# Kernel tuning notes

Measured on AMD Instinct MI355X. Metric: run time of the kernel, lower is better.

The kernel has to match this reference:

```python
import jax, jax.numpy as jnp
import numpy as np

D = 384
MAXPOS = 6

def setup_inputs() -> dict:
    key = jax.random.key(0)
    ks = jax.random.split(key, 20)
    B, Lt, Lh, E = 4, 1024, 512, 64
    inp = {
        'text': jax.random.normal(ks[0], (B, Lt, D), jnp.float32),
        'html': jax.random.normal(ks[1], (B, Lh, D), jnp.float32),
        'H2Hmask': jax.random.randint(ks[2], (B, Lh, Lh), 0, E, jnp.int32),
        'T2Tmask': (jax.random.uniform(ks[3], (B, Lt, Lt)) < 0.1).astype(jnp.float32),
        'H2Tmask': (jax.random.uniform(ks[4], (B, Lh, Lt)) < 0.1).astype(jnp.float32),
        'T2Hmask': (jax.random.uniform(ks[5], (B, Lt, Lh)) < 0.1).astype(jnp.float32),
        'positionembedding': jax.random.normal(ks[6], (2 * MAXPOS + 1, D), jnp.float32) * 0.02,
        'htmledgeembedding': jax.random.normal(ks[7], (E, D), jnp.float32) * 0.02,
    }
    names = ['W_V_T', 'W_V_H', 'W_Q_H2H', 'W_K_H2H', 'W_Q_H2T', 'W_K_H2T',
             'W_Q_T2H', 'W_K_T2H', 'W_Q_T2T', 'W_K_T2T']
    lim = np.sqrt(6.0 / (D + D))  # glorot_uniform
    for i, n in enumerate(names):
        inp[n] = jax.random.uniform(ks[8 + i], (D, D), jnp.float32, -lim, lim)
    return inp


def _forward(text, html, H2Hmask, T2Tmask, H2Tmask, T2Hmask,
             positionembedding, htmledgeembedding,
             W_V_T, W_V_H, W_Q_H2H, W_K_H2H, W_Q_H2T, W_K_H2T,
             W_Q_T2H, W_K_T2H, W_Q_T2T, W_K_T2T):
    B, Lt, _ = text.shape
    Lh = html.shape[1]
    scale = 1.0 / jnp.sqrt(jnp.float32(D))

    text_v = text @ W_V_T   # (B,Lt,D)
    html_v = html @ W_V_H   # (B,Lh,D)

    # ---- H2H: content + gathered edge-embedding bias ----
    # sum_d q[b,i,d] * (k[b,j,d] + edge[H2Hmask[b,i,j], d])
    #   = (q k^T)[b,i,j] + (q E^T)[b,i, H2Hmask[b,i,j]]
    h2h_q = html @ W_Q_H2H
    h2h_k = html @ W_K_H2H
    h2h_content = jnp.einsum('bid,bjd->bij', h2h_q, h2h_k)
    qe = h2h_q @ htmledgeembedding.T                       # (B,Lh,E)
    h2h_bias = jnp.take_along_axis(qe, H2Hmask, axis=-1)   # (B,Lh,Lh)
    h2h_e = (h2h_content + h2h_bias) * scale
    h2h_e = h2h_e - 10000.0 * (H2Hmask == 0).astype(jnp.float32)
    html1 = jax.nn.softmax(h2h_e, axis=-1) @ html_v

    # ---- H2T ----
    h2t_e = jnp.einsum('bid,bjd->bij', html @ W_Q_H2T, text @ W_K_H2T) * scale
    h2t_e = h2t_e - 10000.0 * H2Tmask
    html2 = jax.nn.softmax(h2t_e, axis=-1) @ text_v

    # ---- T2H (note: original code never applies T2Hmask) ----
    t2h_e = jnp.einsum('bid,bjd->bij', text @ W_Q_T2H, html @ W_K_T2H) * scale
    text1 = jax.nn.softmax(t2h_e, axis=-1) @ html_v

    # ---- T2T: content + relative-position bias ----
    idx = jnp.arange(Lt, dtype=jnp.int32)
    pos_ids = jnp.clip(idx[None, :] - idx[:, None], -MAXPOS, MAXPOS) + MAXPOS  # (Lt,Lt)
    t2t_q = text @ W_Q_T2T
    t2t_k = text @ W_K_T2T
    t2t_content = jnp.einsum('bid,bjd->bij', t2t_q, t2t_k)
    qp = t2t_q @ positionembedding.T                       # (B,Lt,2*MAXPOS+1)
    t2t_bias = jnp.take_along_axis(
        qp, jnp.broadcast_to(pos_ids[None], (B, Lt, Lt)), axis=-1)
    t2t_e = (t2t_content + t2t_bias) * scale
    t2t_e = t2t_e - 10000.0 * T2Tmask
    text2 = jax.nn.softmax(t2t_e, axis=-1) @ text_v

    # concat updated text (Lt) and html (Lh) along seq axis -> (B, Lt+Lh, D)
    return jnp.concatenate([text1 + text2, html1 + html2], axis=1)


def reference(text, html, H2Hmask, T2Tmask, H2Tmask, T2Hmask,
              positionembedding, htmledgeembedding,
              W_V_T, W_V_H, W_Q_H2H, W_K_H2H, W_Q_H2T, W_K_H2T,
              W_Q_T2H, W_K_T2H, W_Q_T2T, W_K_T2T):
    return _forward(text, html, H2Hmask, T2Tmask, H2Tmask, T2Hmask,
                    positionembedding, htmledgeembedding,
                    W_V_T, W_V_H, W_Q_H2H, W_K_H2H, W_Q_H2T, W_K_H2T,
                    W_Q_T2H, W_K_T2H, W_Q_T2T, W_K_T2T)
```

## Files before the change

### kernel.cpp

```cpp
#include <hip/hip_runtime.h>
#include <math.h>

typedef unsigned short u16;
typedef unsigned int u32;
typedef __attribute__((ext_vector_type(8))) short short8;
typedef __attribute__((ext_vector_type(4))) float f32x4;

__device__ __forceinline__ u16 f2bf(float f) {
    u32 u = __float_as_uint(f);
    u = (u + 0x7FFFu + ((u >> 16) & 1u)) >> 16;
    return (u16)u;
}
__device__ __forceinline__ float bf2f(u16 h) {
    return __uint_as_float(((u32)h) << 16);
}
__device__ __forceinline__ float4 ld4f(const float* p) {
    return *reinterpret_cast<const float4*>(p);
}


__global__ __launch_bounds__(256)
void cvt2(const float4* __restrict__ a, int na4,
          const float4* __restrict__ b, int nb4,
          u16* __restrict__ oa, u16* __restrict__ ob)
{
    int idx = blockIdx.x * 256 + threadIdx.x;
    const int tot = na4 + nb4;
    for (; idx < tot; idx += gridDim.x * 256) {
        float4 v; u16* o;
        if (idx < na4) { v = a[idx];        o = oa + (long)idx * 4; }
        else           { v = b[idx - na4];  o = ob + (long)(idx - na4) * 4; }
        u32 lo = (u32)f2bf(v.x) | ((u32)f2bf(v.y) << 16);
        u32 hi = (u32)f2bf(v.z) | ((u32)f2bf(v.w) << 16);
        uint2 pk; pk.x = lo; pk.y = hi;
        *reinterpret_cast<uint2*>(o) = pk;
    }
}

struct WP { const float* p[10]; };
struct WD { u16* d[10]; };

__global__ __launch_bounds__(1024)
void wtrans(WP w, WD wd)
{
    __shared__ float t[32][33];
    const int z = blockIdx.z;
    const float* W = w.p[z];
    const int k = blockIdx.x * 32 + threadIdx.y;
    const int n = blockIdx.y * 32 + threadIdx.x;
    t[threadIdx.y][threadIdx.x] = W[k * 384 + n];
    __syncthreads();
    const int no = blockIdx.y * 32 + threadIdx.y;
    const int ko = blockIdx.x * 32 + threadIdx.x;
    wd.d[z][no * 384 + ko] = f2bf(t[threadIdx.x][threadIdx.y]);
}

__device__ __forceinline__ void mfma_core64(
    const u16* __restrict__ A, int lda,
    const u16* __restrict__ B, int ldb, int K,
    u16 (&As)[2][4096], u16 (&Bs)[2][4096],
    f32x4 (&acc)[2][2])
{
    const int tid  = threadIdx.x;
    const int wid  = tid >> 6;
    const int lane = tid & 63;
    const int wr = wid >> 1, wc = wid & 1;
    const int lane15 = lane & 15;
    const int lq = lane >> 4;
    const int g0 = wid * 64 + lane;

    #pragma unroll
    for (int i = 0; i < 2; ++i)
        #pragma unroll
        for (int j = 0; j < 2; ++j)
            acc[i][j] = (f32x4){0.f, 0.f, 0.f, 0.f};

    auto stage = [&](const u16* __restrict__ G, int ld, int k0, u16* lds) {
        #pragma unroll
        for (int h = 0; h < 2; ++h) {
            const int gid  = g0 + h * 256;
            const int row  = gid >> 3;
            const int slot = (gid & 7) ^ (row & 7);
            const u16* src = G + (long)row * ld + k0 + slot * 8;
            u16* dst = lds + wid * 512 + h * 2048;
            __builtin_amdgcn_global_load_lds(
                (const __attribute__((address_space(1))) void*)src,
                (__attribute__((address_space(3))) void*)dst, 16, 0, 0);
        }
    };
    auto rd = [&](const u16* lds, int row, int colslot) -> short8 {
        const int byt = row * 128 + ((colslot ^ (row & 7)) << 4);
        return *reinterpret_cast<const short8*>(
            reinterpret_cast<const char*>(lds) + byt);
    };

    stage(A, lda, 0, As[0]);
    stage(B, ldb, 0, Bs[0]);
    __syncthreads();

    const int nt = K >> 6;
    int cur = 0;
    for (int t = 0; t < nt; ++t) {
        if (t + 1 < nt) {
            stage(A, lda, (t + 1) << 6, As[cur ^ 1]);
            stage(B, ldb, (t + 1) << 6, Bs[cur ^ 1]);
        }
        short8 af[2][2], bf[2][2];
        #pragma unroll
        for (int mi = 0; mi < 2; ++mi)
            #pragma unroll
            for (int kk = 0; kk < 2; ++kk)
                af[mi][kk] = rd(As[cur], wr * 32 + mi * 16 + lane15, kk * 4 + lq);
        #pragma unroll
        for (int ni = 0; ni < 2; ++ni)
            #pragma unroll
            for (int kk = 0; kk < 2; ++kk)
                bf[ni][kk] = rd(Bs[cur], wc * 32 + ni * 16 + lane15, kk * 4 + lq);
        #pragma unroll
        for (int mi = 0; mi < 2; ++mi)
            #pragma unroll
            for (int ni = 0; ni < 2; ++ni)
                #pragma unroll
                for (int kk = 0; kk < 2; ++kk)
                    acc[mi][ni] = __builtin_amdgcn_mfma_f32_16x16x32_bf16(
                        af[mi][kk], bf[ni][kk], acc[mi][ni], 0, 0, 0);
        __syncthreads();
        cur ^= 1;
    }
}

struct Seg {
    const u16* A; const u16* B; float* C;
    long sA, sB, sC;
    int lda, ldb, ldc, K, nbx, nbxSh, start, pad;
};
struct Segs { Seg s[4]; };

template<int NSEG>
__global__ __launch_bounds__(256)
void gemm_grouped(Segs d)
{
    __shared__ __align__(16) u16 As[2][4096];
    __shared__ __align__(16) u16 Bs[2][4096];
    const int bid = blockIdx.x;
    Seg sg = d.s[0];
    if (NSEG > 1 && bid >= d.s[1].start) sg = d.s[1];
    if (NSEG > 2 && bid >= d.s[2].start) sg = d.s[2];
    if (NSEG > 3 && bid >= d.s[3].start) sg = d.s[3];

    const int local = bid - sg.start;
    const int bx = local & (sg.nbx - 1);
    const int by = local >> sg.nbxSh;
    const int z  = blockIdx.y;
    const int m0 = bx * 64, n0 = by * 64;

    const u16* A = sg.A + (long)z * sg.sA + (long)m0 * sg.lda;
    const u16* B = sg.B + (long)z * sg.sB + (long)n0 * sg.ldb;

    f32x4 acc[2][2];
    mfma_core64(A, sg.lda, B, sg.ldb, sg.K, As, Bs, acc);

    const int tid = threadIdx.x;
    const int wid = tid >> 6, lane = tid & 63;
    const int wr = wid >> 1, wc = wid & 1;
    const int lane15 = lane & 15;
    const int r0 = (lane >> 4) * 4;

    float* C = sg.C + (long)z * sg.sC;
    #pragma unroll
    for (int mi = 0; mi < 2; ++mi)
        #pragma unroll
        for (int r = 0; r < 4; ++r) {
            const int row = m0 + wr * 32 + mi * 16 + r0 + r;
            float* crow = C + (long)row * sg.ldc + n0 + wc * 32 + lane15;
            #pragma unroll
            for (int ni = 0; ni < 2; ++ni)
                crow[ni * 16] = acc[mi][ni][r];
        }
}

struct PSeg {
    const u16* A; const u16* Bw; u16* QK; u16* VT;
    int lvtSh, vtOff, nbx, nbxSh, start, pad;
};
struct PSegs { PSeg s[2]; };

__global__ __launch_bounds__(256)
void proj_grouped(PSegs d)
{
    __shared__ __align__(16) u16 As[2][4096];
    __shared__ __align__(16) u16 Bs[2][4096];
    const int bid = blockIdx.x;
    PSeg sg = d.s[0];
    if (bid >= d.s[1].start) sg = d.s[1];

    const int local = bid - sg.start;
    const int bx = local & (sg.nbx - 1);
    const int by = local >> sg.nbxSh;
    const int m0 = bx * 64, n0 = by * 64;

    const u16* A = sg.A + (long)m0 * 384;
    const u16* B = sg.Bw + (long)n0 * 384;

    f32x4 acc[2][2];
    mfma_core64(A, 384, B, 384, 384, As, Bs, acc);

    const int tid = threadIdx.x;
    const int wid = tid >> 6, lane = tid & 63;
    const int wr = wid >> 1, wc = wid & 1;
    const int lane15 = lane & 15;
    const int r0 = (lane >> 4) * 4;
    const int lmask = (1 << sg.lvtSh) - 1;

    if (n0 < 384) {
        #pragma unroll
        for (int mi = 0; mi < 2; ++mi) {
            const int row = m0 + wr * 32 + mi * 16 + r0;
            const int bz = row >> sg.lvtSh;
            const int l  = row & lmask;
            #pragma unroll
            for (int ni = 0; ni < 2; ++ni) {
                const int col = n0 + wc * 32 + ni * 16 + lane15;
                u32 lo = (u32)f2bf(acc[mi][ni][0]) | ((u32)f2bf(acc[mi][ni][1]) << 16);
                u32 hi = (u32)f2bf(acc[mi][ni][2]) | ((u32)f2bf(acc[mi][ni][3]) << 16);
                uint2 pk; pk.x = lo; pk.y = hi;
                *reinterpret_cast<uint2*>(
                    sg.VT + ((long)bz * 384 + col) * 1536 + sg.vtOff + l) = pk;
            }
        }
    } else {
        #pragma unroll
        for (int mi = 0; mi < 2; ++mi)
            #pragma unroll
            for (int r = 0; r < 4; ++r) {
                const int row = m0 + wr * 32 + mi * 16 + r0 + r;
                u16* qrow = sg.QK + (long)row * 1536 + (n0 - 384) + wc * 32 + lane15;
                #pragma unroll
                for (int ni = 0; ni < 2; ++ni)
                    qrow[ni * 16] = f2bf(acc[mi][ni][r]);
            }
    }
}

__global__ __launch_bounds__(256)
void gemm_bias2(const u16* __restrict__ A0, const float* __restrict__ B0,
                float* __restrict__ C0, int N0,
                const u16* __restrict__ A1, const float* __restrict__ B1,
                float* __restrict__ C1, int N1)
{
    __shared__ float As[16][64];
    __shared__ float Bs[16][64];
    const int bid = blockIdx.x;
    const u16* A; const float* B; float* C; int N, m0;
    if (bid < 32) { A = A0; B = B0; C = C0; N = N0; m0 = bid * 64; }
    else          { A = A1; B = B1; C = C1; N = N1; m0 = (bid - 32) * 64; }

    const int tid = threadIdx.x;
    const int tx = tid & 15, ty = tid >> 4;
    const int ar = tid >> 2;
    const int ak = (tid & 3) << 2;

    float acc[4][4] = {{0.f,0.f,0.f,0.f},{0.f,0.f,0.f,0.f},
                       {0.f,0.f,0.f,0.f},{0.f,0.f,0.f,0.f}};

    for (int k0 = 0; k0 < 384; k0 += 16) {
        const u16* ap = A + (long)(m0 + ar) * 1536 + (k0 + ak);
        ushort4 a4 = *reinterpret_cast<const ushort4*>(ap);
        As[ak+0][ar] = bf2f(a4.x); As[ak+1][ar] = bf2f(a4.y);
        As[ak+2][ar] = bf2f(a4.z); As[ak+3][ar] = bf2f(a4.w);

        float4 bv = make_float4(0.f,0.f,0.f,0.f);
        if (ar < N) bv = ld4f(B + (long)ar * 384 + (k0 + ak));
        Bs[ak+0][ar] = bv.x; Bs[ak+1][ar] = bv.y;
        Bs[ak+2][ar] = bv.z; Bs[ak+3][ar] = bv.w;
        __syncthreads();

        #pragma unroll
        for (int kk = 0; kk < 16; ++kk) {
            float4 af = ld4f(&As[kk][ty * 4]);
            float4 bfv = ld4f(&Bs[kk][tx * 4]);
            float a[4] = {af.x, af.y, af.z, af.w};
            float b[4] = {bfv.x, bfv.y, bfv.z, bfv.w};
            #pragma unroll
            for (int i = 0; i < 4; ++i)
                #pragma unroll
                for (int j = 0; j < 4; ++j)
                    acc[i][j] = fmaf(a[i], b[j], acc[i][j]);
        }
        __syncthreads();
    }
    #pragma unroll
    for (int i = 0; i < 4; ++i) {
        const int row = m0 + ty * 4 + i;
        float* crow = C + (long)row * N;
        #pragma unroll
        for (int j = 0; j < 4; ++j) {
            const int col = tx * 4 + j;
            if (col < N) crow[col] = acc[i][j];
        }
    }
}


__device__ __forceinline__ float blockReduceMax(float v, float* red, int tid) {
    #pragma unroll
    for (int o = 32; o >= 1; o >>= 1) v = fmaxf(v, __shfl_xor(v, o));
    if ((tid & 63) == 0) red[tid >> 6] = v;
    __syncthreads();
    return fmaxf(fmaxf(red[0], red[1]), fmaxf(red[2], red[3]));
}
__device__ __forceinline__ float blockReduceSum(float v, float* red, int tid) {
    #pragma unroll
    for (int o = 32; o >= 1; o >>= 1) v += __shfl_xor(v, o);
    if ((tid & 63) == 0) red[4 + (tid >> 6)] = v;
    __syncthreads();
    return red[4] + red[5] + red[6] + red[7];
}

__global__ __launch_bounds__(256)
void softmax_fused(const float* __restrict__ scoresH, u16* __restrict__ probsH,
                   const float* __restrict__ scoresT, u16* __restrict__ probsT,
                   const float* __restrict__ qe, const float* __restrict__ qp,
                   const int* __restrict__ H2Hmask,
                   const float* __restrict__ H2Tmask,
                   const float* __restrict__ T2Tmask, float scale)
{
    const int bid = blockIdx.x;
    const int tid = threadIdx.x;
    __shared__ float qsh[64];
    __shared__ float red[8];

    if (bid < 2048) {
        const int b = bid >> 9, i = bid & 511;
        const long rbase = ((long)b * 512 + i) * 1536;
        const float* rowS = scoresH + rbase;
        u16* rowP = probsH + rbase;
        const int*   mrow  = H2Hmask + ((long)b * 512 + i) * 512;
        const float* m2row = H2Tmask + ((long)b * 512 + i) * 1024;
        if (tid < 64) qsh[tid] = qe[((long)b * 512 + i) * 64 + tid];
        __syncthreads();

        float x[2]; float mx = -1e30f;
        #pragma unroll
        for (int t = 0; t < 2; ++t) {
            const int j = tid + t * 256;
            const int m = mrow[j];
            float v = (rowS[j] + qsh[m]) * scale - 10000.f * (m == 0 ? 1.f : 0.f);
            x[t] = v; mx = fmaxf(mx, v);
        }
        mx = blockReduceMax(mx, red, tid);
        float s = 0.f;
        #pragma unroll
        for (int t = 0; t < 2; ++t) { x[t] = __expf(x[t] - mx); s += x[t]; }
        s = blockReduceSum(s, red, tid);
        float inv = 1.f / s;
        #pragma unroll
        for (int t = 0; t < 2; ++t) rowP[tid + t * 256] = f2bf(x[t] * inv);

        float y[4]; mx = -1e30f;
        #pragma unroll
        for (int t = 0; t < 4; ++t) {
            const int jj = tid + t * 256;
            float v = rowS[512 + jj] * scale - 10000.f * m2row[jj];
            y[t] = v; mx = fmaxf(mx, v);
        }
        mx = blockReduceMax(mx, red, tid);
        s = 0.f;
        #pragma unroll
        for (int t = 0; t < 4; ++t) { y[t] = __expf(y[t] - mx); s += y[t]; }
        s = blockReduceSum(s, red, tid);
        inv = 1.f / s;
        #pragma unroll
        for (int t = 0; t < 4; ++t) rowP[512 + tid + t * 256] = f2bf(y[t] * inv);
    } else {
        const int bid2 = bid - 2048;
        const int b = bid2 >> 10, i = bid2 & 1023;
        const long rbase = ((long)b * 1024 + i) * 1536;
        const float* rowS = scoresT + rbase;
        u16* rowP = probsT + rbase;
        const float* m2row = T2Tmask + ((long)b * 1024 + i) * 1024;
        if (tid < 13) qsh[tid] = qp[((long)b * 1024 + i) * 13 + tid];
        __syncthreads();

        float x[2]; float mx = -1e30f;
        #pragma unroll
        for (int t = 0; t < 2; ++t) {
            const int j = tid + t * 256;
            float v = rowS[j] * scale;
            x[t] = v; mx = fmaxf(mx, v);
        }
        mx = blockReduceMax(mx, red, tid);
        float s = 0.f;
        #pragma unroll
        for (int t = 0; t < 2; ++t) { x[t] = __expf(x[t] - mx); s += x[t]; }
        s = blockReduceSum(s, red, tid);
        float inv = 1.f / s;
        #pragma unroll
        for (int t = 0; t < 2; ++t) rowP[tid + t * 256] = f2bf(x[t] * inv);

        float y[4]; mx = -1e30f;
        #pragma unroll
        for (int t = 0; t < 4; ++t) {
            const int jj = tid + t * 256;
            int pos = jj - i;
            pos = (pos < -6 ? -6 : (pos > 6 ? 6 : pos)) + 6;
            float v = (rowS[512 + jj] + qsh[pos]) * scale - 10000.f * m2row[jj];
            y[t] = v; mx = fmaxf(mx, v);
        }
        mx = blockReduceMax(mx, red, tid);
        s = 0.f;
        #pragma unroll
        for (int t = 0; t < 4; ++t) { y[t] = __expf(y[t] - mx); s += y[t]; }
        s = blockReduceSum(s, red, tid);
        inv = 1.f / s;
        #pragma unroll
        for (int t = 0; t < 4; ++t) rowP[512 + tid + t * 256] = f2bf(y[t] * inv);
    }
}


extern "C" void kernel_launch(void* const* d_in, const int* in_sizes, int n_in,
                              void* d_out, int out_size, void* d_ws, size_t ws_size,
                              hipStream_t stream)
{
    const int Bn = 4, Lt = 1024, Lh = 512, Dd = 384;
    const float scale = 0.05103103630798288f;

    const float* text    = (const float*)d_in[0];
    const float* html    = (const float*)d_in[1];
    const int*   H2Hmask = (const int*)  d_in[2];
    const float* T2Tmask = (const float*)d_in[3];
    const float* H2Tmask = (const float*)d_in[4];
    const float* posemb  = (const float*)d_in[6];
    const float* edgeemb = (const float*)d_in[7];
    float* out = (float*)d_out;

    char* p = (char*)d_ws;
    auto au16 = [&](long n) { u16* r = (u16*)p;  p += ((n * 2 + 255) & ~255L); return r; };
    auto af32 = [&](long n) { float* r = (float*)p; p += ((n * 4 + 255) & ~255L); return r; };

    const long nT = (long)Bn * Lt * Dd;
    const long nH = (long)Bn * Lh * Dd;
    u16* text_bf = au16(nT);
    u16* html_bf = au16(nH);
    u16* WTtext  = au16(5L * 384 * 384);
    u16* WThtml  = au16(5L * 384 * 384);
    u16* textQK  = au16((long)Bn * Lt * 1536);
    u16* htmlQK  = au16((long)Bn * Lh * 1536);
    u16* VTs     = au16((long)Bn * 384 * 1536);
    float* qe = af32((long)Bn * Lh * 64);
    float* qp = af32((long)Bn * Lt * 13);
    float* scoresH = af32((long)Bn * Lh * 1536);
    float* scoresT = af32((long)Bn * Lt * 1536);
    u16* probsH = au16((long)Bn * Lh * 1536);
    u16* probsT = au16((long)Bn * Lt * 1536);

    cvt2<<<2048, 256, 0, stream>>>((const float4*)text, (int)(nT / 4),
                                   (const float4*)html, (int)(nH / 4),
                                   text_bf, html_bf);
    WP wp; WD wd;
    for (int i = 0; i < 10; ++i) wp.p[i] = (const float*)d_in[8 + i];
    const long WSZ = 147456;
    wd.d[0] = WTtext + 0 * WSZ;
    wd.d[1] = WThtml + 0 * WSZ;
    wd.d[2] = WThtml + 1 * WSZ;
    wd.d[3] = WThtml + 2 * WSZ;
    wd.d[4] = WThtml + 3 * WSZ;
    wd.d[5] = WTtext + 1 * WSZ;
    wd.d[6] = WTtext + 2 * WSZ;
    wd.d[7] = WThtml + 4 * WSZ;
    wd.d[8] = WTtext + 3 * WSZ;
    wd.d[9] = WTtext + 4 * WSZ;
    wtrans<<<dim3(12, 12, 10), dim3(32, 32), 0, stream>>>(wp, wd);

    u16* h2h_q = htmlQK + 0;     u16* h2h_k = htmlQK + 384;
    u16* h2t_q = htmlQK + 768;   u16* t2h_k = htmlQK + 1152;
    u16* h2t_k = textQK + 0;     u16* t2h_q = textQK + 384;
    u16* t2t_q = textQK + 768;   u16* t2t_k = textQK + 1152;

    PSegs pj;
    pj.s[0] = { text_bf, WTtext, textQK, VTs, 10, 512, 64, 6, 0,    0 };
    pj.s[1] = { html_bf, WThtml, htmlQK, VTs,  9,   0, 32, 5, 1920, 0 };
    proj_grouped<<<2880, 256, 0, stream>>>(pj);

    gemm_bias2<<<96, 256, 0, stream>>>(h2h_q, edgeemb, qe, 64,
                                       t2t_q, posemb,  qp, 13);

    const long sQt = (long)Lt * 1536, sQh = (long)Lh * 1536;
    const long sSh = (long)Lh * 1536, sSt = (long)Lt * 1536;
    const long sV  = (long)384 * 1536;
    const long sOut = (long)(Lt + Lh) * 384;

    Segs sc;
    sc.s[0] = { h2h_q, h2h_k, scoresH,       sQh, sQh, sSh, 1536, 1536, 1536, 384,  8, 3,   0, 0 };
    sc.s[1] = { h2t_q, h2t_k, scoresH + 512, sQh, sQt, sSh, 1536, 1536, 1536, 384,  8, 3,  64, 0 };
    sc.s[2] = { t2h_q, t2h_k, scoresT,       sQt, sQh, sSt, 1536, 1536, 1536, 384, 16, 4, 192, 0 };
    sc.s[3] = { t2t_q, t2t_k, scoresT + 512, sQt, sQt, sSt, 1536, 1536, 1536, 384, 16, 4, 320, 0 };
    gemm_grouped<4><<<dim3(576, 4), 256, 0, stream>>>(sc);

    softmax_fused<<<6144, 256, 0, stream>>>(scoresH, probsH, scoresT, probsT,
                                            qe, qp, H2Hmask, H2Tmask, T2Tmask,
                                            scale);

    Segs pv;
    pv.s[0] = { probsH, VTs, out + (long)Lt * 384, sQh, sV, sOut, 1536, 1536, 384, 1536,  8, 3,  0, 0 };
    pv.s[1] = { probsT, VTs, out,                  sQt, sV, sOut, 1536, 1536, 384, 1536, 16, 4, 48, 0 };
    pv.s[2] = pv.s[1]; pv.s[3] = pv.s[1];
    gemm_grouped<2><<<dim3(144, 4), 256, 0, stream>>>(pv);
}
```

Before: 215.9 us.

## Use 128x128 MFMA tiles and fold bias GEMMs into grouped score GEMM

The MFMA GEMM core moves from 64x64 tiles with a double-buffered, XOR-swizzled K=64 pipeline to 128x128 tiles with a single-buffered K=32 loop. Each wave now computes 4x4 fragments, which raises arithmetic intensity per LDS load. The separate scalar-FMA gemm_bias2 kernel is removed. The edge and position embeddings are converted to bf16 and padded to 128 rows, and the q·E^T and q·P^T products run as two extra segments of the grouped score GEMM. This cuts one launch and reuses the tensor-core path, but drops the load/compute overlap and leaves LDS reads unswizzled, so bank conflicts are likely. It also launches far fewer blocks, which may underfill the GPU.

```diff
diff --git a/kernel.cpp b/kernel.cpp
--- a/kernel.cpp
+++ b/kernel.cpp
@@ -14,22 +14,25 @@
 __device__ __forceinline__ float bf2f(u16 h) {
     return __uint_as_float(((u32)h) << 16);
 }
-__device__ __forceinline__ float4 ld4f(const float* p) {
-    return *reinterpret_cast<const float4*>(p);
-}
 
 
 __global__ __launch_bounds__(256)
-void cvt2(const float4* __restrict__ a, int na4,
+void cvt4(const float4* __restrict__ a, int na4,
           const float4* __restrict__ b, int nb4,
-          u16* __restrict__ oa, u16* __restrict__ ob)
+          const float4* __restrict__ c, int nc4,
+          const float4* __restrict__ d, int nd4,
+          u16* __restrict__ oa, u16* __restrict__ ob,
+          u16* __restrict__ oc, u16* __restrict__ od)
 {
     int idx = blockIdx.x * 256 + threadIdx.x;
-    const int tot = na4 + nb4;
+    const int tot = na4 + nb4 + nc4 + nd4;
     for (; idx < tot; idx += gridDim.x * 256) {
         float4 v; u16* o;
-        if (idx < na4) { v = a[idx];        o = oa + (long)idx * 4; }
-        else           { v = b[idx - na4];  o = ob + (long)(idx - na4) * 4; }
+        int t = idx;
+        if (t < na4)      { v = a[t]; o = oa + (long)t * 4; }
+        else if ((t -= na4) < nb4) { v = b[t]; o = ob + (long)t * 4; }
+        else if ((t -= nb4) < nc4) { v = c[t]; o = oc + (long)t * 4; }
+        else { t -= nc4;    v = d[t]; o = od + (long)t * 4; }
         u32 lo = (u32)f2bf(v.x) | ((u32)f2bf(v.y) << 16);
         u32 hi = (u32)f2bf(v.z) | ((u32)f2bf(v.w) << 16);
         uint2 pk; pk.x = lo; pk.y = hi;
@@ -55,77 +58,60 @@
     wd.d[z][no * 384 + ko] = f2bf(t[threadIdx.x][threadIdx.y]);
 }
 
-__device__ __forceinline__ void mfma_core64(
+__device__ __forceinline__ void mfma_core128(
     const u16* __restrict__ A, int lda,
     const u16* __restrict__ B, int ldb, int K,
-    u16 (&As)[2][4096], u16 (&Bs)[2][4096],
-    f32x4 (&acc)[2][2])
+    u16* __restrict__ As, u16* __restrict__ Bs,
+    f32x4 (&acc)[4][4])
 {
     const int tid  = threadIdx.x;
     const int wid  = tid >> 6;
     const int lane = tid & 63;
     const int wr = wid >> 1, wc = wid & 1;
     const int lane15 = lane & 15;
-    const int lq = lane >> 4;
-    const int g0 = wid * 64 + lane;
+    const int kg = (lane >> 4) * 8;
+    const int srow = lane >> 2;
+    const int scol = (lane & 3) * 8;
 
     #pragma unroll
-    for (int i = 0; i < 2; ++i)
-        #pragma unroll
-        for (int j = 0; j < 2; ++j)
+    for (int i = 0; i < 4; ++i)
+        #pragma unroll
+        for (int j = 0; j < 4; ++j)
             acc[i][j] = (f32x4){0.f, 0.f, 0.f, 0.f};
 
-    auto stage = [&](const u16* __restrict__ G, int ld, int k0, u16* lds) {
-        #pragma unroll
-        for (int h = 0; h < 2; ++h) {
-            const int gid  = g0 + h * 256;
-            const int row  = gid >> 3;
-            const int slot = (gid & 7) ^ (row & 7);
-            const u16* src = G + (long)row * ld + k0 + slot * 8;
-            u16* dst = lds + wid * 512 + h * 2048;
+    for (int k0 = 0; k0 < K; k0 += 32) {
+        #pragma unroll
+        for (int i = 0; i < 2; ++i) {
+            const int rg = (wid * 2 + i) * 16;
+            const u16* ga = A + (long)(rg + srow) * lda + (k0 + scol);
+            const u16* gb = B + (long)(rg + srow) * ldb + (k0 + scol);
+            u16* la = As + (wid * 2 + i) * 512;
+            u16* lb = Bs + (wid * 2 + i) * 512;
             __builtin_amdgcn_global_load_lds(
-                (const __attribute__((address_space(1))) void*)src,
-                (__attribute__((address_space(3))) void*)dst, 16, 0, 0);
-        }
-    };
-    auto rd = [&](const u16* lds, int row, int colslot) -> short8 {
-        const int byt = row * 128 + ((colslot ^ (row & 7)) << 4);
-        return *reinterpret_cast<const short8*>(
-            reinterpret_cast<const char*>(lds) + byt);
-    };
-
-    stage(A, lda, 0, As[0]);
-    stage(B, ldb, 0, Bs[0]);
-    __syncthreads();
-
-    const int nt = K >> 6;
-    int cur = 0;
-    for (int t = 0; t < nt; ++t) {
-        if (t + 1 < nt) {
-            stage(A, lda, (t + 1) << 6, As[cur ^ 1]);
-            stage(B, ldb, (t + 1) << 6, Bs[cur ^ 1]);
-        }
-        short8 af[2][2], bf[2][2];
-        #pragma unroll
-        for (int mi = 0; mi < 2; ++mi)
+                (const __attribute__((address_space(1))) void*)ga,
+                (__attribute__((address_space(3))) void*)la, 16, 0, 0);
+            __builtin_amdgcn_global_load_lds(
+                (const __attribute__((address_space(1))) void*)gb,
+                (__attribute__((address_space(3))) void*)lb, 16, 0, 0);
+        }
+        __syncthreads();
+
+        short8 af[4], bf[4];
+        #pragma unroll
+        for (int mi = 0; mi < 4; ++mi)
+            af[mi] = *reinterpret_cast<const short8*>(
+                As + (wr * 64 + mi * 16 + lane15) * 32 + kg);
+        #pragma unroll
+        for (int ni = 0; ni < 4; ++ni)
+            bf[ni] = *reinterpret_cast<const short8*>(
+                Bs + (wc * 64 + ni * 16 + lane15) * 32 + kg);
+        #pragma unroll
+        for (int mi = 0; mi < 4; ++mi)
             #pragma unroll
-            for (int kk = 0; kk < 2; ++kk)
-                af[mi][kk] = rd(As[cur], wr * 32 + mi * 16 + lane15, kk * 4 + lq);
-        #pragma unroll
-        for (int ni = 0; ni < 2; ++ni)
-            #pragma unroll
-            for (int kk = 0; kk < 2; ++kk)
-                bf[ni][kk] = rd(Bs[cur], wc * 32 + ni * 16 + lane15, kk * 4 + lq);
-        #pragma unroll
-        for (int mi = 0; mi < 2; ++mi)
-            #pragma unroll
-            for (int ni = 0; ni < 2; ++ni)
-                #pragma unroll
-                for (int kk = 0; kk < 2; ++kk)
-                    acc[mi][ni] = __builtin_amdgcn_mfma_f32_16x16x32_bf16(
-                        af[mi][kk], bf[ni][kk], acc[mi][ni], 0, 0, 0);
+            for (int ni = 0; ni < 4; ++ni)
+                acc[mi][ni] = __builtin_amdgcn_mfma_f32_16x16x32_bf16(
+                    af[mi], bf[ni], acc[mi][ni], 0, 0, 0);
         __syncthreads();
-        cur ^= 1;
     }
 }
 
@@ -134,31 +120,33 @@
     long sA, sB, sC;
     int lda, ldb, ldc, K, nbx, nbxSh, start, pad;
 };
-struct Segs { Seg s[4]; };
+struct Segs { Seg s[6]; };
 
 template<int NSEG>
 __global__ __launch_bounds__(256)
 void gemm_grouped(Segs d)
 {
-    __shared__ __align__(16) u16 As[2][4096];
-    __shared__ __align__(16) u16 Bs[2][4096];
+    __shared__ __align__(16) u16 As[4096];
+    __shared__ __align__(16) u16 Bs[4096];
     const int bid = blockIdx.x;
     Seg sg = d.s[0];
     if (NSEG > 1 && bid >= d.s[1].start) sg = d.s[1];
     if (NSEG > 2 && bid >= d.s[2].start) sg = d.s[2];
     if (NSEG > 3 && bid >= d.s[3].start) sg = d.s[3];
+    if (NSEG > 4 && bid >= d.s[4].start) sg = d.s[4];
+    if (NSEG > 5 && bid >= d.s[5].start) sg = d.s[5];
 
     const int local = bid - sg.start;
     const int bx = local & (sg.nbx - 1);
     const int by = local >> sg.nbxSh;
     const int z  = blockIdx.y;
-    const int m0 = bx * 64, n0 = by * 64;
+    const int m0 = bx * 128, n0 = by * 128;
 
     const u16* A = sg.A + (long)z * sg.sA + (long)m0 * sg.lda;
     const u16* B = sg.B + (long)z * sg.sB + (long)n0 * sg.ldb;
 
-    f32x4 acc[2][2];
-    mfma_core64(A, sg.lda, B, sg.ldb, sg.K, As, Bs, acc);
+    f32x4 acc[4][4];
+    mfma_core128(A, sg.lda, B, sg.ldb, sg.K, As, Bs, acc);
 
     const int tid = threadIdx.x;
     const int wid = tid >> 6, lane = tid & 63;
@@ -168,13 +156,13 @@
 
     float* C = sg.C + (long)z * sg.sC;
     #pragma unroll
-    for (int mi = 0; mi < 2; ++mi)
+    for (int mi = 0; mi < 4; ++mi)
         #pragma unroll
         for (int r = 0; r < 4; ++r) {
-            const int row = m0 + wr * 32 + mi * 16 + r0 + r;
-            float* crow = C + (long)row * sg.ldc + n0 + wc * 32 + lane15;
+            const int row = m0 + wr * 64 + mi * 16 + r0 + r;
+            float* crow = C + (long)row * sg.ldc + n0 + wc * 64 + lane15;
             #pragma unroll
-            for (int ni = 0; ni < 2; ++ni)
+            for (int ni = 0; ni < 4; ++ni)
                 crow[ni * 16] = acc[mi][ni][r];
         }
 }
@@ -188,8 +176,8 @@
 __global__ __launch_bounds__(256)
 void proj_grouped(PSegs d)
 {
-    __shared__ __align__(16) u16 As[2][4096];
-    __shared__ __align__(16) u16 Bs[2][4096];
+    __shared__ __align__(16) u16 As[4096];
+    __shared__ __align__(16) u16 Bs[4096];
     const int bid = blockIdx.x;
     PSeg sg = d.s[0];
     if (bid >= d.s[1].start) sg = d.s[1];
@@ -197,13 +185,13 @@
     const int local = bid - sg.start;
     const int bx = local & (sg.nbx - 1);
     const int by = local >> sg.nbxSh;
-    const int m0 = bx * 64, n0 = by * 64;
+    const int m0 = bx * 128, n0 = by * 128;
 
     const u16* A = sg.A + (long)m0 * 384;
     const u16* B = sg.Bw + (long)n0 * 384;
 
-    f32x4 acc[2][2];
-    mfma_core64(A, 384, B, 384, 384, As, Bs, acc);
+    f32x4 acc[4][4];
+    mfma_core128(A, 384, B, 384, 384, As, Bs, acc);
 
     const int tid = threadIdx.x;
     const int wid = tid >> 6, lane = tid & 63;
@@ -214,13 +202,13 @@
 
     if (n0 < 384) {
         #pragma unroll
-        for (int mi = 0; mi < 2; ++mi) {
-            const int row = m0 + wr * 32 + mi * 16 + r0;
+        for (int mi = 0; mi < 4; ++mi) {
+            const int row = m0 + wr * 64 + mi * 16 + r0;
             const int bz = row >> sg.lvtSh;
             const int l  = row & lmask;
             #pragma unroll
-            for (int ni = 0; ni < 2; ++ni) {
-                const int col = n0 + wc * 32 + ni * 16 + lane15;
+            for (int ni = 0; ni < 4; ++ni) {
+                const int col = n0 + wc * 64 + ni * 16 + lane15;
                 u32 lo = (u32)f2bf(acc[mi][ni][0]) | ((u32)f2bf(acc[mi][ni][1]) << 16);
                 u32 hi = (u32)f2bf(acc[mi][ni][2]) | ((u32)f2bf(acc[mi][ni][3]) << 16);
                 uint2 pk; pk.x = lo; pk.y = hi;
@@ -230,74 +218,15 @@
         }
     } else {
         #pragma unroll
-        for (int mi = 0; mi < 2; ++mi)
+        for (int mi = 0; mi < 4; ++mi)
             #pragma unroll
             for (int r = 0; r < 4; ++r) {
-                const int row = m0 + wr * 32 + mi * 16 + r0 + r;
-                u16* qrow = sg.QK + (long)row * 1536 + (n0 - 384) + wc * 32 + lane15;
+                const int row = m0 + wr * 64 + mi * 16 + r0 + r;
+                u16* qrow = sg.QK + (long)row * 1536 + (n0 - 384) + wc * 64 + lane15;
                 #pragma unroll
-                for (int ni = 0; ni < 2; ++ni)
+                for (int ni = 0; ni < 4; ++ni)
                     qrow[ni * 16] = f2bf(acc[mi][ni][r]);
             }
-    }
-}
-
-__global__ __launch_bounds__(256)
-void gemm_bias2(const u16* __restrict__ A0, const float* __restrict__ B0,
-                float* __restrict__ C0, int N0,
-                const u16* __restrict__ A1, const float* __restrict__ B1,
-                float* __restrict__ C1, int N1)
-{
-    __shared__ float As[16][64];
-    __shared__ float Bs[16][64];
-    const int bid = blockIdx.x;
-    const u16* A; const float* B; float* C; int N, m0;
-    if (bid < 32) { A = A0; B = B0; C = C0; N = N0; m0 = bid * 64; }
-    else          { A = A1; B = B1; C = C1; N = N1; m0 = (bid - 32) * 64; }
-
-    const int tid = threadIdx.x;
-    const int tx = tid & 15, ty = tid >> 4;
-    const int ar = tid >> 2;
-    const int ak = (tid & 3) << 2;
-
-    float acc[4][4] = {{0.f,0.f,0.f,0.f},{0.f,0.f,0.f,0.f},
-                       {0.f,0.f,0.f,0.f},{0.f,0.f,0.f,0.f}};
-
-    for (int k0 = 0; k0 < 384; k0 += 16) {
-        const u16* ap = A + (long)(m0 + ar) * 1536 + (k0 + ak);
-        ushort4 a4 = *reinterpret_cast<const ushort4*>(ap);
-        As[ak+0][ar] = bf2f(a4.x); As[ak+1][ar] = bf2f(a4.y);
-        As[ak+2][ar] = bf2f(a4.z); As[ak+3][ar] = bf2f(a4.w);
-
-        float4 bv = make_float4(0.f,0.f,0.f,0.f);
-        if (ar < N) bv = ld4f(B + (long)ar * 384 + (k0 + ak));
-        Bs[ak+0][ar] = bv.x; Bs[ak+1][ar] = bv.y;
-        Bs[ak+2][ar] = bv.z; Bs[ak+3][ar] = bv.w;
-        __syncthreads();
-
-        #pragma unroll
-        for (int kk = 0; kk < 16; ++kk) {
-            float4 af = ld4f(&As[kk][ty * 4]);
-            float4 bfv = ld4f(&Bs[kk][tx * 4]);
-            float a[4] = {af.x, af.y, af.z, af.w};
-            float b[4] = {bfv.x, bfv.y, bfv.z, bfv.w};
-            #pragma unroll
-            for (int i = 0; i < 4; ++i)
-                #pragma unroll
-                for (int j = 0; j < 4; ++j)
-                    acc[i][j] = fmaf(a[i], b[j], acc[i][j]);
-        }
-        __syncthreads();
-    }
-    #pragma unroll
-    for (int i = 0; i < 4; ++i) {
-        const int row = m0 + ty * 4 + i;
-        float* crow = C + (long)row * N;
-        #pragma unroll
-        for (int j = 0; j < 4; ++j) {
-            const int col = tx * 4 + j;
-            if (col < N) crow[col] = acc[i][j];
-        }
     }
 }
 
@@ -337,7 +266,7 @@
         u16* rowP = probsH + rbase;
         const int*   mrow  = H2Hmask + ((long)b * 512 + i) * 512;
         const float* m2row = H2Tmask + ((long)b * 512 + i) * 1024;
-        if (tid < 64) qsh[tid] = qe[((long)b * 512 + i) * 64 + tid];
+        if (tid < 64) qsh[tid] = qe[((long)b * 512 + i) * 128 + tid];
         __syncthreads();
 
         float x[2]; float mx = -1e30f;
@@ -379,7 +308,7 @@
         const float* rowS = scoresT + rbase;
         u16* rowP = probsT + rbase;
         const float* m2row = T2Tmask + ((long)b * 1024 + i) * 1024;
-        if (tid < 13) qsh[tid] = qp[((long)b * 1024 + i) * 13 + tid];
+        if (tid < 13) qsh[tid] = qp[((long)b * 1024 + i) * 128 + tid];
         __syncthreads();
 
         float x[2]; float mx = -1e30f;
@@ -423,7 +352,7 @@
                               void* d_out, int out_size, void* d_ws, size_t ws_size,
                               hipStream_t stream)
 {
-    const int Bn = 4, Lt = 1024, Lh = 512, Dd = 384;
+    const int Bn = 4, Lt = 1024, Lh = 512;
     const float scale = 0.05103103630798288f;
 
     const float* text    = (const float*)d_in[0];
@@ -439,25 +368,29 @@
     auto au16 = [&](long n) { u16* r = (u16*)p;  p += ((n * 2 + 255) & ~255L); return r; };
     auto af32 = [&](long n) { float* r = (float*)p; p += ((n * 4 + 255) & ~255L); return r; };
 
-    const long nT = (long)Bn * Lt * Dd;
-    const long nH = (long)Bn * Lh * Dd;
+    const long nT = (long)Bn * Lt * 384;
+    const long nH = (long)Bn * Lh * 384;
     u16* text_bf = au16(nT);
     u16* html_bf = au16(nH);
     u16* WTtext  = au16(5L * 384 * 384);
     u16* WThtml  = au16(5L * 384 * 384);
+    u16* edge_bf = au16(128L * 384);
+    u16* pos_bf  = au16(128L * 384);
     u16* textQK  = au16((long)Bn * Lt * 1536);
     u16* htmlQK  = au16((long)Bn * Lh * 1536);
     u16* VTs     = au16((long)Bn * 384 * 1536);
-    float* qe = af32((long)Bn * Lh * 64);
-    float* qp = af32((long)Bn * Lt * 13);
+    float* qe = af32((long)Bn * Lh * 128);
+    float* qp = af32((long)Bn * Lt * 128);
     float* scoresH = af32((long)Bn * Lh * 1536);
     float* scoresT = af32((long)Bn * Lt * 1536);
     u16* probsH = au16((long)Bn * Lh * 1536);
     u16* probsT = au16((long)Bn * Lt * 1536);
 
-    cvt2<<<2048, 256, 0, stream>>>((const float4*)text, (int)(nT / 4),
+    cvt4<<<2048, 256, 0, stream>>>((const float4*)text, (int)(nT / 4),
                                    (const float4*)html, (int)(nH / 4),
-                                   text_bf, html_bf);
+                                   (const float4*)edgeemb, 64 * 384 / 4,
+                                   (const float4*)posemb, 13 * 384 / 4,
+                                   text_bf, html_bf, edge_bf, pos_bf);
     WP wp; WD wd;
     for (int i = 0; i < 10; ++i) wp.p[i] = (const float*)d_in[8 + i];
     const long WSZ = 147456;
@@ -479,12 +412,9 @@
     u16* t2t_q = textQK + 768;   u16* t2t_k = textQK + 1152;
 
     PSegs pj;
-    pj.s[0] = { text_bf, WTtext, textQK, VTs, 10, 512, 64, 6, 0,    0 };
-    pj.s[1] = { html_bf, WThtml, htmlQK, VTs,  9,   0, 32, 5, 1920, 0 };
-    proj_grouped<<<2880, 256, 0, stream>>>(pj);
-
-    gemm_bias2<<<96, 256, 0, stream>>>(h2h_q, edgeemb, qe, 64,
-                                       t2t_q, posemb,  qp, 13);
+    pj.s[0] = { text_bf, WTtext, textQK, VTs, 10, 512, 32, 5, 0,   0 };
+    pj.s[1] = { html_bf, WThtml, htmlQK, VTs,  9,   0, 16, 4, 480, 0 };
+    proj_grouped<<<720, 256, 0, stream>>>(pj);
 
     const long sQt = (long)Lt * 1536, sQh = (long)Lh * 1536;
     const long sSh = (long)Lh * 1536, sSt = (long)Lt * 1536;
@@ -492,19 +422,21 @@
     const long sOut = (long)(Lt + Lh) * 384;
 
     Segs sc;
-    sc.s[0] = { h2h_q, h2h_k, scoresH,       sQh, sQh, sSh, 1536, 1536, 1536, 384,  8, 3,   0, 0 };
-    sc.s[1] = { h2t_q, h2t_k, scoresH + 512, sQh, sQt, sSh, 1536, 1536, 1536, 384,  8, 3,  64, 0 };
-    sc.s[2] = { t2h_q, t2h_k, scoresT,       sQt, sQh, sSt, 1536, 1536, 1536, 384, 16, 4, 192, 0 };
-    sc.s[3] = { t2t_q, t2t_k, scoresT + 512, sQt, sQt, sSt, 1536, 1536, 1536, 384, 16, 4, 320, 0 };
-    gemm_grouped<4><<<dim3(576, 4), 256, 0, stream>>>(sc);
+    sc.s[0] = { h2h_q, h2h_k,  scoresH,       sQh, sQh, sSh, 1536, 1536, 1536, 384, 4, 2,   0, 0 };
+    sc.s[1] = { h2t_q, h2t_k,  scoresH + 512, sQh, sQt, sSh, 1536, 1536, 1536, 384, 4, 2,  16, 0 };
+    sc.s[2] = { t2h_q, t2h_k,  scoresT,       sQt, sQh, sSt, 1536, 1536, 1536, 384, 8, 3,  48, 0 };
+    sc.s[3] = { t2t_q, t2t_k,  scoresT + 512, sQt, sQt, sSt, 1536, 1536, 1536, 384, 8, 3,  80, 0 };
+    sc.s[4] = { h2h_q, edge_bf, qe,           sQh, 0,   (long)Lh * 128, 1536, 384, 128, 384, 4, 2, 144, 0 };
+    sc.s[5] = { t2t_q, pos_bf,  qp,           sQt, 0,   (long)Lt * 128, 1536, 384, 128, 384, 8, 3, 148, 0 };
+    gemm_grouped<6><<<dim3(156, 4), 256, 0, stream>>>(sc);
 
     softmax_fused<<<6144, 256, 0, stream>>>(scoresH, probsH, scoresT, probsT,
                                             qe, qp, H2Hmask, H2Tmask, T2Tmask,
                                             scale);
 
     Segs pv;
-    pv.s[0] = { probsH, VTs, out + (long)Lt * 384, sQh, sV, sOut, 1536, 1536, 384, 1536,  8, 3,  0, 0 };
-    pv.s[1] = { probsT, VTs, out,                  sQt, sV, sOut, 1536, 1536, 384, 1536, 16, 4, 48, 0 };
-    pv.s[2] = pv.s[1]; pv.s[3] = pv.s[1];
-    gemm_grouped<2><<<dim3(144, 4), 256, 0, stream>>>(pv);
-}
+    pv.s[0] = { probsH, VTs, out + (long)Lt * 384, sQh, sV, sOut, 1536, 1536, 384, 1536, 4, 2,  0, 0 };
+    pv.s[1] = { probsT, VTs, out,                  sQt, sV, sOut, 1536, 1536, 384, 1536, 8, 3, 12, 0 };
+    pv.s[2] = pv.s[1]; pv.s[3] = pv.s[1]; pv.s[4] = pv.s[1]; pv.s[5] = pv.s[1];
+    gemm_grouped<2><<<dim3(36, 4), 256, 0, stream>>>(pv);
+}
```

New measurement: 209.6 us. 3.0% less time.
